# Optimization experiments

Hardware: AMD Instinct MI355X
Metric: run time of the kernel (lower is better)

Reference implementation:

```python
import jax, jax.numpy as jnp
import numpy as np

D = 1024
E = 8
K = 2
NUM_ITER = 2
DT = 0.1
H = 64           # controller_hidden
CTX = 2 * D


def _gelu(t):
    return jax.nn.gelu(t, approximate=False)


def _inl(ctrl, x, v, mu):
    # ctrl: [T, 3D] -> alpha, beta, gate chunks of size D
    alpha_raw, beta_raw, gate_raw = jnp.split(ctrl, 3, axis=-1)
    alpha = jax.nn.sigmoid(alpha_raw)
    beta = jax.nn.softplus(beta_raw)
    gate = jax.nn.sigmoid(gate_raw)
    error = x - mu
    v_next = alpha * v - beta * error
    x_next = x + DT * gate * v_next
    return x_next, v_next


def setup_inputs() -> dict:
    key = jax.random.key(0)
    ks = jax.random.split(key, 20)
    s = 0.02
    inp = {
        'x': jax.random.normal(ks[0], (4, 4096, D), jnp.float32),
        # router MLP
        'w_r1': jax.random.normal(ks[1], (D, D // 4), jnp.float32) * s,
        'b_r1': jnp.zeros((D // 4,), jnp.float32),
        'w_r2': jax.random.normal(ks[2], (D // 4, E), jnp.float32) * s,
        'b_r2': jnp.zeros((E,), jnp.float32),
        # halt gate MLP
        'w_h1': jax.random.normal(ks[3], (D, D // 4), jnp.float32) * s,
        'b_h1': jnp.zeros((D // 4,), jnp.float32),
        'w_h2': jax.random.normal(ks[4], (D // 4, 1), jnp.float32) * s,
        'b_h2': jnp.zeros((1,), jnp.float32),
        # expert tables
        'expert_w1': jax.random.normal(ks[5], (E, CTX, H), jnp.float32) * s,
        'expert_b1': jnp.zeros((E, H), jnp.float32),
        'expert_w2': jax.random.normal(ks[6], (E, H, 3 * D), jnp.float32) * s,
        'expert_b2': jnp.zeros((E, 3 * D), jnp.float32),
        # shared expert
        'w_s1': jax.random.normal(ks[7], (CTX, H), jnp.float32) * s,
        'b_s1': jnp.zeros((H,), jnp.float32),
        'w_s2': jax.random.normal(ks[8], (H, 3 * D), jnp.float32) * s,
        'b_s2': jnp.zeros((3 * D,), jnp.float32),
        'shared_weight': jnp.asarray(0.5, jnp.float32),
        # refine MLP
        'w_f1': jax.random.normal(ks[9], (D, 2 * D), jnp.float32) * s,
        'b_f1': jnp.zeros((2 * D,), jnp.float32),
        'w_f2': jax.random.normal(ks[10], (2 * D, D), jnp.float32) * s,
        'b_f2': jnp.zeros((D,), jnp.float32),
        'integration_weight': jnp.full((D,), 0.5, jnp.float32),
        'mu': jnp.zeros((D,), jnp.float32),
    }
    return inp


def reference(x, w_r1, b_r1, w_r2, b_r2, w_h1, b_h1, w_h2, b_h2,
              expert_w1, expert_b1, expert_w2, expert_b2,
              w_s1, b_s1, w_s2, b_s2, shared_weight,
              w_f1, b_f1, w_f2, b_f2, integration_weight, mu):
    B, N, Dm = x.shape
    xf = x.reshape(B * N, Dm)                       # [T, D]

    # router: top-k over softmax probs, renormalized
    logits = _gelu(xf @ w_r1 + b_r1) @ w_r2 + b_r2  # [T, E]
    probs = jax.nn.softmax(logits, axis=-1)
    top_p, top_i = jax.lax.top_k(probs, K)          # [T, K]
    top_p = top_p / jnp.sum(top_p, axis=-1, keepdims=True)

    flat_idx = top_i.reshape(-1)                    # [T*K]
    flat_w = top_p.reshape(-1, 1)                   # [T*K, 1]

    v = jnp.zeros_like(xf)
    integrated = xf
    for _ in range(NUM_ITER):
        ctx = jnp.concatenate([integrated, v], axis=-1)     # [T, 2D]

        # shared expert path
        shared_ctrl = _gelu(ctx @ w_s1 + b_s1) @ w_s2 + b_s2
        x_shared, v_shared = _inl(shared_ctrl, integrated, v, mu)
        sw = jax.nn.sigmoid(shared_weight)

        # routed experts: gather per-token weights, per-token matvec
        ctx_e = jnp.repeat(ctx, K, axis=0)                  # [T*K, 2D]
        x_e = jnp.repeat(integrated, K, axis=0)
        v_e = jnp.repeat(v, K, axis=0)
        w1 = expert_w1[flat_idx]                            # [T*K, 2D, H]
        b1 = expert_b1[flat_idx]
        w2 = expert_w2[flat_idx]                            # [T*K, H, 3D]
        b2 = expert_b2[flat_idx]
        hidden = _gelu(jnp.einsum('tc,tch->th', ctx_e, w1) + b1)
        ctrl = jnp.einsum('th,tho->to', hidden, w2) + b2    # [T*K, 3D]
        x_r, v_r = _inl(ctrl, x_e, v_e, mu)
        x_r = (x_r * flat_w).reshape(B * N, K, Dm).sum(axis=1)
        v_r = (v_r * flat_w).reshape(B * N, K, Dm).sum(axis=1)

        x_next = sw * x_shared + (1.0 - sw) * x_r
        v_next = sw * v_shared + (1.0 - sw) * v_r

        halt = jax.nn.sigmoid(_gelu(x_next @ w_h1 + b_h1) @ w_h2 + b_h2)  # [T,1]
        refined = _gelu(x_next @ w_f1 + b_f1) @ w_f2 + b_f2               # [T,D]
        integrated = integrated + halt * refined * integration_weight
        v = v_next

    return integrated.reshape(B, N, Dm)
```

## Files before the change

kernel.cpp:

```cpp
#include <hip/hip_runtime.h>


#define TOK   16384
#define DDIM  1024
#define NEXP  8
#define DTC   0.1f
#define NDESC 160

using f32x4 = __attribute__((ext_vector_type(4))) float;
using bfv8  = __attribute__((ext_vector_type(8))) short;

__device__ __forceinline__ unsigned short f2bf(float x){
  unsigned u = __builtin_bit_cast(unsigned, x);
  u += 0x7fffu + ((u >> 16) & 1u);
  return (unsigned short)(u >> 16);
}
__device__ __forceinline__ float bf2f(unsigned short h){
  return __builtin_bit_cast(float, ((unsigned)h) << 16);
}
__device__ __forceinline__ float geluf(float x){
  return 0.5f * x * (1.0f + erff(x * 0.7071067811865476f));
}
__device__ __forceinline__ float sigmf(float x){ return 1.0f/(1.0f+__expf(-x)); }
__device__ __forceinline__ float softpf(float x){
  return fmaxf(x, 0.0f) + __logf(1.0f + __expf(-fabsf(x)));
}
__device__ __forceinline__ f32x4 mfma16(bfv8 a, bfv8 b, f32x4 c){
  return __builtin_amdgcn_mfma_f32_16x16x32_bf16(a, b, c, 0, 0, 0);
}
typedef __attribute__((address_space(1))) const void gvoid_t;
typedef __attribute__((address_space(3))) void svoid_t;
__device__ __forceinline__ void gload16(const void* g, void* l){
  __builtin_amdgcn_global_load_lds((gvoid_t*)g, (svoid_t*)l, 16, 0, 0);
}

__global__ __launch_bounds__(256) void transpose_cast(
    const float* __restrict__ src, unsigned short* __restrict__ dst, int R, int C)
{
  __shared__ float tile[32][33];
  size_t bo = (size_t)blockIdx.z * R * C;
  const float* s = src + bo;
  unsigned short* d = dst + bo;
  int c0 = blockIdx.x * 32, r0 = blockIdx.y * 32;
  int tx = threadIdx.x, ty = threadIdx.y;
  #pragma unroll
  for (int j = 0; j < 4; j++)
    tile[ty + 8*j][tx] = s[(size_t)(r0 + ty + 8*j) * C + c0 + tx];
  __syncthreads();
  #pragma unroll
  for (int j = 0; j < 4; j++)
    d[(size_t)(c0 + ty + 8*j) * R + r0 + tx] = f2bf(tile[tx][ty + 8*j]);
}

__global__ __launch_bounds__(256) void ctx_k(
    const float* __restrict__ outf, unsigned short* __restrict__ ctx)
{
  const int n = TOK * 256;
  for (int i = blockIdx.x * 256 + threadIdx.x; i < n; i += gridDim.x * 256) {
    int t = i >> 8, c4 = (i & 255) * 4;
    float4 xi = ((const float4*)outf)[i];
    ushort4 xb = {f2bf(xi.x), f2bf(xi.y), f2bf(xi.z), f2bf(xi.w)};
    *(ushort4*)&ctx[(size_t)t*2048 + c4] = xb;
    *(ushort4*)&ctx[(size_t)t*2048 + 1024 + c4] = ushort4{0,0,0,0};
  }
}

template<int EPI>
__global__ __launch_bounds__(256) void gemm_k(
    const unsigned short* __restrict__ A, int lda,
    const unsigned short* __restrict__ BT,
    const float* __restrict__ bias, const float* __restrict__ bias2,
    int Kd, int N,
    unsigned short* __restrict__ obf, unsigned short* __restrict__ obf2,
    const float* __restrict__ halt, const float* __restrict__ iw,
    float* __restrict__ integ, unsigned short* __restrict__ ctxX)
{
  __shared__ unsigned short As[128][64];
  __shared__ unsigned short Bs[128][64];
  const int total = gridDim.x * gridDim.y;
  const int bid = blockIdx.y * gridDim.x + blockIdx.x;
  const int swz = (bid & 7) * (total >> 3) + (bid >> 3);
  const int bx = swz % gridDim.x, by = swz / gridDim.x;

  const int tid  = threadIdx.x, lane = tid & 63, w = tid >> 6;
  const int wm   = w >> 1, wn = w & 1;
  const int gm0  = by * 128, gn0 = bx * 128;
  const int r8   = lane >> 3;
  const int sseg = (lane & 7) ^ r8;

  const unsigned short* aga[4];
  const unsigned short* bga[4];
  #pragma unroll
  for (int c = 0; c < 4; c++) {
    aga[c] = A  + (size_t)(gm0 + w*32 + c*8 + r8) * lda + sseg*8;
    bga[c] = BT + (size_t)(gn0 + w*32 + c*8 + r8) * Kd  + sseg*8;
  }

  f32x4 acc[4][4];
  #pragma unroll
  for (int i = 0; i < 4; i++)
    #pragma unroll
    for (int j = 0; j < 4; j++)
      acc[i][j] = f32x4{0.f,0.f,0.f,0.f};

  const int xr = (lane & 7) << 3;
  for (int k0 = 0; k0 < Kd; k0 += 64) {
    #pragma unroll
    for (int c = 0; c < 4; c++) gload16(aga[c] + k0, &As[w*32 + c*8][0]);
    #pragma unroll
    for (int c = 0; c < 4; c++) gload16(bga[c] + k0, &Bs[w*32 + c*8][0]);
    __syncthreads();
    #pragma unroll
    for (int kk = 0; kk < 64; kk += 32) {
      const int kof = kk + ((lane >> 4) << 3);
      bfv8 a[4], b[4];
      #pragma unroll
      for (int mf = 0; mf < 4; mf++)
        a[mf] = *(const bfv8*)&As[wm*64 + mf*16 + (lane & 15)][kof ^ xr];
      #pragma unroll
      for (int nf = 0; nf < 4; nf++)
        b[nf] = *(const bfv8*)&Bs[wn*64 + nf*16 + (lane & 15)][kof ^ xr];
      #pragma unroll
      for (int mf = 0; mf < 4; mf++)
        #pragma unroll
        for (int nf = 0; nf < 4; nf++)
          acc[mf][nf] = mfma16(a[mf], b[nf], acc[mf][nf]);
    }
    __syncthreads();
  }

  #pragma unroll
  for (int mf = 0; mf < 4; mf++) {
    #pragma unroll
    for (int nf = 0; nf < 4; nf++) {
      int col = gn0 + wn*64 + nf*16 + (lane & 15);
      float bc;
      if (EPI == 2) bc = (col < 2048) ? bias[col] : bias2[col - 2048];
      else          bc = bias[col];
      #pragma unroll
      for (int r = 0; r < 4; r++) {
        int row = gm0 + wm*64 + mf*16 + ((lane >> 4) << 2) + r;
        float v = acc[mf][nf][r] + bc;
        if (EPI == 0) {
          obf[(size_t)row * N + col] = f2bf(geluf(v));
        } else if (EPI == 2) {
          if (col < 2048) obf [(size_t)row * 2048 + col]        = f2bf(geluf(v));
          else            obf2[(size_t)row * 256 + (col - 2048)] = f2bf(geluf(v));
        } else {
          size_t ix = (size_t)row * DDIM + col;
          float nv = integ[ix] + halt[row] * v * iw[col];
          integ[ix] = nv;
          ctxX[(size_t)row * 2048 + col] = f2bf(nv);
        }
      }
    }
  }
}

__global__ __launch_bounds__(256) void router_k(
    const unsigned short* __restrict__ h1, const float* __restrict__ w_r2,
    const float* __restrict__ b_r2, int* __restrict__ topi, float* __restrict__ topw)
{
  int t = blockIdx.x * 4 + (threadIdx.x >> 6);
  int lane = threadIdx.x & 63;
  const unsigned short* hp = h1 + (size_t)t * 256 + lane * 4;
  float hv[4];
  #pragma unroll
  for (int j = 0; j < 4; j++) hv[j] = bf2f(hp[j]);
  float acc[8];
  #pragma unroll
  for (int e = 0; e < 8; e++) acc[e] = 0.f;
  #pragma unroll
  for (int j = 0; j < 4; j++) {
    const float* wr = w_r2 + (size_t)(lane*4 + j) * 8;
    #pragma unroll
    for (int e = 0; e < 8; e++) acc[e] += hv[j] * wr[e];
  }
  #pragma unroll
  for (int off = 32; off > 0; off >>= 1)
    #pragma unroll
    for (int e = 0; e < 8; e++) acc[e] += __shfl_xor(acc[e], off);
  if (lane == 0) {
    float lg[8];
    #pragma unroll
    for (int e = 0; e < 8; e++) lg[e] = acc[e] + b_r2[e];
    int i0 = 0; float m0 = lg[0];
    #pragma unroll
    for (int e = 1; e < 8; e++) if (lg[e] > m0) { m0 = lg[e]; i0 = e; }
    int i1 = -1; float m1 = -3.4e38f;
    #pragma unroll
    for (int e = 0; e < 8; e++) if (e != i0 && lg[e] > m1) { m1 = lg[e]; i1 = e; }
    float w0 = 1.0f / (1.0f + expf(m1 - m0));
    topi[t*2] = i0; topi[t*2+1] = i1;
    topw[t*2] = w0; topw[t*2+1] = 1.0f - w0;
  }
}

__global__ __launch_bounds__(256) void haltgate_k(
    const unsigned short* __restrict__ h1, const float* __restrict__ w_h2,
    const float* __restrict__ b_h2, float* __restrict__ halt)
{
  int t = blockIdx.x * 4 + (threadIdx.x >> 6);
  int lane = threadIdx.x & 63;
  const unsigned short* hp = h1 + (size_t)t * 256 + lane * 4;
  float s = 0.f;
  #pragma unroll
  for (int j = 0; j < 4; j++) s += bf2f(hp[j]) * w_h2[lane*4 + j];
  #pragma unroll
  for (int off = 32; off > 0; off >>= 1) s += __shfl_xor(s, off);
  if (lane == 0) halt[t] = sigmf(s + b_h2[0]);
}

__global__ __launch_bounds__(256) void pairb_k(
    const int* __restrict__ topi, const float* __restrict__ topw,
    int* __restrict__ cnt, int* __restrict__ plist, float* __restrict__ wA)
{
  int t = blockIdx.x * 256 + threadIdx.x;
  int a = topi[2*t], b = topi[2*t+1];
  float wa = topw[2*t];
  if (a > b) { int tmp = a; a = b; b = tmp; wa = 1.0f - wa; }
  int pid = a * 8 + b;
  int pos = atomicAdd(&cnt[pid], 1);
  plist[pid * TOK + pos] = t;
  wA[t] = wa;
}

__global__ void desc_k(const int* __restrict__ cnt, int4* __restrict__ desc,
                       int* __restrict__ ndesc)
{
  if (threadIdx.x == 0 && blockIdx.x == 0) {
    int nt = 0, hb = 0;
    for (int p = 0; p < 64; p++) {
      int c = cnt[p];
      for (int o = 0; o < c; o += 128) {
        int rem = c - o; if (rem > 128) rem = 128;
        desc[nt] = make_int4(p, o, rem, hb);
        nt++; hb += 384;
      }
    }
    ndesc[0] = nt;
  }
}

__global__ __launch_bounds__(256) void exp1p_k(
    const unsigned short* __restrict__ ctx,
    const int4* __restrict__ desc, const int* __restrict__ ndesc,
    const int* __restrict__ plist,
    const unsigned short* __restrict__ ew1T, const float* __restrict__ eb1,
    const unsigned short* __restrict__ ws1T, const float* __restrict__ bs1,
    unsigned short* __restrict__ hiddenG)
{
  __shared__ unsigned short As[128][64];
  __shared__ unsigned short Bs[64][64];
  __shared__ int s_tok[128];
  if (blockIdx.x >= ndesc[0]) return;
  int4 dd = desc[blockIdx.x];
  const int pid = dd.x, goff = dd.y, cnt = dd.z, hbase = dd.w;
  const int path = blockIdx.y;
  const int ep = (path == 0) ? (pid >> 3) : (pid & 7);
  const unsigned short* w1 = (path < 2) ? ew1T + (size_t)ep * 64 * 2048 : ws1T;
  const float* b1 = (path < 2) ? eb1 + ep * 64 : bs1;
  const int tid = threadIdx.x, lane = tid & 63, w = tid >> 6;

  if (tid < 128)
    s_tok[tid] = (tid < cnt) ? plist[pid * TOK + goff + tid] : 0;
  __syncthreads();

  const int arow = w*8 + (lane >> 3);
  const int sseg = (lane & 7) ^ (lane >> 3);
  const unsigned short* asrc[4];
  #pragma unroll
  for (int q = 0; q < 4; q++)
    asrc[q] = ctx + (size_t)s_tok[q*32 + arow] * 2048 + sseg * 8;
  const unsigned short* bsrc[2];
  #pragma unroll
  for (int q = 0; q < 2; q++)
    bsrc[q] = w1 + (size_t)(q*32 + arow) * 2048 + sseg * 8;

  f32x4 acc[2][4];
  #pragma unroll
  for (int i = 0; i < 2; i++)
    #pragma unroll
    for (int j = 0; j < 4; j++)
      acc[i][j] = f32x4{0.f,0.f,0.f,0.f};

  const int xr = (lane & 7) << 3;
  for (int k0 = 0; k0 < 2048; k0 += 64) {
    #pragma unroll
    for (int q = 0; q < 4; q++) gload16(asrc[q] + k0, &As[q*32 + w*8][0]);
    #pragma unroll
    for (int q = 0; q < 2; q++) gload16(bsrc[q] + k0, &Bs[q*32 + w*8][0]);
    __syncthreads();
    #pragma unroll
    for (int kk = 0; kk < 64; kk += 32) {
      const int kof = kk + ((lane >> 4) << 3);
      bfv8 a[2], b[4];
      #pragma unroll
      for (int mf = 0; mf < 2; mf++)
        a[mf] = *(const bfv8*)&As[w*32 + mf*16 + (lane & 15)][kof ^ xr];
      #pragma unroll
      for (int nf = 0; nf < 4; nf++)
        b[nf] = *(const bfv8*)&Bs[nf*16 + (lane & 15)][kof ^ xr];
      #pragma unroll
      for (int mf = 0; mf < 2; mf++)
        #pragma unroll
        for (int nf = 0; nf < 4; nf++)
          acc[mf][nf] = mfma16(a[mf], b[nf], acc[mf][nf]);
    }
    __syncthreads();
  }

  #pragma unroll
  for (int mf = 0; mf < 2; mf++) {
    #pragma unroll
    for (int nf = 0; nf < 4; nf++) {
      int col = nf*16 + (lane & 15);
      float bb = b1[col];
      #pragma unroll
      for (int r = 0; r < 4; r++) {
        int row = w*32 + mf*16 + ((lane >> 4) << 2) + r;
        hiddenG[(size_t)(hbase + path*128 + row) * 64 + col] =
            f2bf(geluf(acc[mf][nf][r] + bb));
      }
    }
  }
}

__global__ __launch_bounds__(256) void exp2p_k(
    const unsigned short* __restrict__ hiddenG,
    const int4* __restrict__ desc, const int* __restrict__ ndesc,
    const int* __restrict__ plist, const float* __restrict__ wA,
    const unsigned short* __restrict__ ew2T, const float* __restrict__ eb2,
    const unsigned short* __restrict__ ws2T, const float* __restrict__ bs2,
    const float* __restrict__ swp, const float* __restrict__ mu,
    unsigned short* __restrict__ ctx, unsigned short* __restrict__ xaccB)
{
  __shared__ unsigned short Hs[192][64];
  __shared__ unsigned short W2s[192][64];
  __shared__ int   s_tok[64];
  __shared__ float s_w[64];
  if (blockIdx.x >= ndesc[0]) return;
  int4 dd = desc[blockIdx.x];
  const int pid = dd.x, goff = dd.y, cnt = dd.z, hbase = dd.w;
  const int rhf = blockIdx.y;
  const int cnth = cnt - rhf * 64;
  if (cnth <= 0) return;
  const int e0 = pid >> 3, e1 = pid & 7;
  const int tid = threadIdx.x, lane = tid & 63, w = tid >> 6;
  const float sw = sigmf(swp[0]);

  if (tid < 64) {
    int gr = rhf*64 + tid;
    int tok = 0; float wa = 0.f;
    if (gr < cnt) { tok = plist[pid * TOK + goff + gr]; wa = wA[tok]; }
    s_tok[tid] = tok; s_w[tid] = wa;
  }
  const int srow = w*8 + (lane >> 3);
  const int sseg = (lane & 7) ^ (lane >> 3);
  #pragma unroll
  for (int q = 0; q < 6; q++) {
    int row = q*32 + srow;
    gload16(hiddenG + (size_t)(hbase + (row >> 6)*128 + rhf*64 + (row & 63))*64 + sseg*8,
            &Hs[q*32 + w*8][0]);
  }
  __syncthreads();

  const int xr = (lane & 7) << 3;
  const unsigned short* w2b[3] = { ew2T + (size_t)e0*3072*64,
                                   ew2T + (size_t)e1*3072*64, ws2T };
  const float* b2b[3] = { eb2 + e0*3072, eb2 + e1*3072, bs2 };

  for (int dcq = 0; dcq < 4; dcq++) {
    const int d00 = blockIdx.z * 256 + dcq * 64;
    float xx[4][4], vv[4][4], vtot[4][4], gvtot[4][4];
    int   toks[4]; float cwa[4];
    #pragma unroll
    for (int r = 0; r < 4; r++) {
      int row = w*16 + ((lane >> 4) << 2) + r;
      toks[r] = s_tok[row]; cwa[r] = s_w[row];
      #pragma unroll
      for (int cf = 0; cf < 4; cf++) {
        int d = d00 + cf*16 + (lane & 15);
        xx[cf][r] = bf2f(ctx[(size_t)toks[r]*2048 + d]);
        vv[cf][r] = bf2f(ctx[(size_t)toks[r]*2048 + 1024 + d]);
        vtot[cf][r] = 0.f; gvtot[cf][r] = 0.f;
      }
    }
    #pragma unroll
    for (int path = 0; path < 3; path++) {
      #pragma unroll
      for (int q = 0; q < 6; q++) {
        int row  = q*32 + srow;
        int grow = (row >> 6)*1024 + d00 + (row & 63);
        gload16(w2b[path] + (size_t)grow*64 + sseg*8, &W2s[q*32 + w*8][0]);
      }
      __syncthreads();
      bfv8 a[2];
      #pragma unroll
      for (int kk = 0; kk < 2; kk++)
        a[kk] = *(const bfv8*)&Hs[path*64 + w*16 + (lane & 15)]
                               [(kk*32 + ((lane >> 4) << 3)) ^ xr];
      f32x4 acc[12];
      #pragma unroll
      for (int j = 0; j < 12; j++) acc[j] = f32x4{0.f,0.f,0.f,0.f};
      #pragma unroll
      for (int kk = 0; kk < 2; kk++) {
        const int kof = kk*32 + ((lane >> 4) << 3);
        #pragma unroll
        for (int nf = 0; nf < 12; nf++) {
          bfv8 b = *(const bfv8*)&W2s[nf*16 + (lane & 15)][kof ^ xr];
          acc[nf] = mfma16(a[kk], b, acc[nf]);
        }
      }
      const float* b2 = b2b[path];
      #pragma unroll
      for (int cf = 0; cf < 4; cf++) {
        int d = d00 + cf*16 + (lane & 15);
        float ba = b2[d], bb = b2[1024 + d], bg = b2[2048 + d];
        float muv = mu[d];
        #pragma unroll
        for (int r = 0; r < 4; r++) {
          float cw = (path == 0) ? (1.f - sw) * cwa[r]
                   : (path == 1) ? (1.f - sw) * (1.f - cwa[r]) : sw;
          float al = sigmf(acc[cf][r] + ba);
          float be = softpf(acc[4 + cf][r] + bb);
          float ga = sigmf(acc[8 + cf][r] + bg);
          float vn = al * vv[cf][r] - be * (xx[cf][r] - muv);
          vtot[cf][r]  += cw * vn;
          gvtot[cf][r] += cw * ga * vn;
        }
      }
      __syncthreads();
    }
    #pragma unroll
    for (int r = 0; r < 4; r++) {
      int row = w*16 + ((lane >> 4) << 2) + r;
      if (row >= cnth) continue;
      int tok = toks[r];
      #pragma unroll
      for (int cf = 0; cf < 4; cf++) {
        int d = d00 + cf*16 + (lane & 15);
        xaccB[(size_t)tok*1024 + d]        = f2bf(xx[cf][r] + DTC * gvtot[cf][r]);
        ctx[(size_t)tok*2048 + 1024 + d]   = f2bf(vtot[cf][r]);
      }
    }
  }
}

extern "C" void kernel_launch(void* const* d_in, const int* in_sizes, int n_in,
                              void* d_out, int out_size, void* d_ws, size_t ws_size,
                              hipStream_t stream)
{
  const float* x    = (const float*)d_in[0];
  const float* w_r1 = (const float*)d_in[1];
  const float* b_r1 = (const float*)d_in[2];
  const float* w_r2 = (const float*)d_in[3];
  const float* b_r2 = (const float*)d_in[4];
  const float* w_h1 = (const float*)d_in[5];
  const float* b_h1 = (const float*)d_in[6];
  const float* w_h2 = (const float*)d_in[7];
  const float* b_h2 = (const float*)d_in[8];
  const float* ew1  = (const float*)d_in[9];
  const float* eb1  = (const float*)d_in[10];
  const float* ew2  = (const float*)d_in[11];
  const float* eb2  = (const float*)d_in[12];
  const float* w_s1 = (const float*)d_in[13];
  const float* b_s1 = (const float*)d_in[14];
  const float* w_s2 = (const float*)d_in[15];
  const float* b_s2 = (const float*)d_in[16];
  const float* swt  = (const float*)d_in[17];
  const float* w_f1 = (const float*)d_in[18];
  const float* b_f1 = (const float*)d_in[19];
  const float* w_f2 = (const float*)d_in[20];
  const float* b_f2 = (const float*)d_in[21];
  const float* iw   = (const float*)d_in[22];
  const float* mu   = (const float*)d_in[23];
  float* out = (float*)d_out;

  char* ws = (char*)d_ws;
  size_t off = 0;
  auto take = [&](size_t bytes) -> char* {
    char* p = ws + off;
    off = (off + bytes + 255) & ~(size_t)255;
    return p;
  };
  const size_t TD4 = (size_t)TOK * DDIM * 4;
  unsigned short* xaccB = (unsigned short*)take((size_t)TOK * 1024 * 2);
  unsigned short* ctx   = (unsigned short*)take((size_t)TOK * 2048 * 2);
  unsigned short* rh    = (unsigned short*)take((size_t)TOK * 2048 * 2);
  unsigned short* hiddenG = (unsigned short*)take((size_t)NDESC * 384 * 64 * 2);
  unsigned short* h1 = (unsigned short*)take((size_t)TOK * 256 * 2);
  float* halt = (float*)take((size_t)TOK * 4);
  int*   topi = (int*)take((size_t)TOK * 2 * 4);
  float* topw = (float*)take((size_t)TOK * 2 * 4);
  int*   cnt  = (int*)take(64 * 4);
  int*   ndsc = (int*)take(64);
  int4*  desc = (int4*)take((size_t)NDESC * 16);
  int*   plist= (int*)take((size_t)64 * TOK * 4);
  float* wAa  = (float*)take((size_t)TOK * 4);
  unsigned short* w_r1T = (unsigned short*)take((size_t)256 * 1024 * 2);
  unsigned short* wFH   = (unsigned short*)take((size_t)2304 * 1024 * 2);
  unsigned short* w_f2T = (unsigned short*)take((size_t)1024 * 2048 * 2);
  unsigned short* w_s1T = (unsigned short*)take((size_t)64 * 2048 * 2);
  unsigned short* w_s2T = (unsigned short*)take((size_t)3072 * 64 * 2);
  unsigned short* ew1T  = (unsigned short*)take((size_t)NEXP * 64 * 2048 * 2);
  unsigned short* ew2T  = (unsigned short*)take((size_t)NEXP * 3072 * 64 * 2);
  if (off > ws_size) return;

  hipMemcpyAsync(out, x, TD4, hipMemcpyDeviceToDevice, stream);
  hipMemsetAsync(cnt, 0, 64 * 4, stream);

  dim3 tb(32, 8);
  transpose_cast<<<dim3(  8, 32, 1), tb, 0, stream>>>(w_r1, w_r1T, 1024,  256);
  transpose_cast<<<dim3( 64, 32, 1), tb, 0, stream>>>(w_f1, wFH, 1024, 2048);
  transpose_cast<<<dim3(  8, 32, 1), tb, 0, stream>>>(w_h1, wFH + (size_t)2048*1024, 1024, 256);
  transpose_cast<<<dim3( 32, 64, 1), tb, 0, stream>>>(w_f2, w_f2T, 2048, 1024);
  transpose_cast<<<dim3(  2, 64, 1), tb, 0, stream>>>(w_s1, w_s1T, 2048,   64);
  transpose_cast<<<dim3( 96,  2, 1), tb, 0, stream>>>(w_s2, w_s2T,   64, 3072);
  transpose_cast<<<dim3(  2, 64, 8), tb, 0, stream>>>(ew1,  ew1T,  2048,   64);
  transpose_cast<<<dim3( 96,  2, 8), tb, 0, stream>>>(ew2,  ew2T,    64, 3072);

  ctx_k<<<2048, 256, 0, stream>>>(out, ctx);
  gemm_k<0><<<dim3(2, 128), 256, 0, stream>>>(
      ctx, 2048, w_r1T, b_r1, nullptr, 1024, 256, h1, nullptr,
      nullptr, nullptr, nullptr, nullptr);
  router_k<<<TOK / 4, 256, 0, stream>>>(h1, w_r2, b_r2, topi, topw);
  pairb_k<<<TOK / 256, 256, 0, stream>>>(topi, topw, cnt, plist, wAa);
  desc_k<<<1, 64, 0, stream>>>(cnt, desc, ndsc);

  for (int it = 0; it < 2; it++) {
    exp1p_k<<<dim3(NDESC, 3), 256, 0, stream>>>(
        ctx, desc, ndsc, plist, ew1T, eb1, w_s1T, b_s1, hiddenG);
    exp2p_k<<<dim3(NDESC, 2, 4), 256, 0, stream>>>(
        hiddenG, desc, ndsc, plist, wAa, ew2T, eb2, w_s2T, b_s2,
        swt, mu, ctx, xaccB);
    gemm_k<2><<<dim3(18, 128), 256, 0, stream>>>(
        xaccB, 1024, wFH, b_f1, b_h1, 1024, 2304, rh, h1,
        nullptr, nullptr, nullptr, nullptr);
    haltgate_k<<<TOK / 4, 256, 0, stream>>>(h1, w_h2, b_h2, halt);
    gemm_k<1><<<dim3(8, 128), 256, 0, stream>>>(
        rh, 2048, w_f2T, b_f2, nullptr, 2048, 1024, nullptr, nullptr,
        halt, iw, out, ctx);
  }
}
```

Before: 1.149 ms.

## Store expert context in pair-grouped padded order and restructure expert kernels

```diff
diff --git a/kernel.cpp b/kernel.cpp
--- a/kernel.cpp
+++ b/kernel.cpp
@@ -5,7 +5,8 @@
 #define DDIM  1024
 #define NEXP  8
 #define DTC   0.1f
-#define NDESC 160
+#define NDESC 320
+#define GPAD  20480
 
 using f32x4 = __attribute__((ext_vector_type(4))) float;
 using bfv8  = __attribute__((ext_vector_type(8))) short;
@@ -52,16 +53,33 @@
     d[(size_t)(c0 + ty + 8*j) * R + r0 + tx] = f2bf(tile[tx][ty + 8*j]);
 }
 
-__global__ __launch_bounds__(256) void ctx_k(
-    const float* __restrict__ outf, unsigned short* __restrict__ ctx)
+__global__ __launch_bounds__(256) void xinit_k(
+    const float* __restrict__ xf, unsigned short* __restrict__ xb)
 {
   const int n = TOK * 256;
   for (int i = blockIdx.x * 256 + threadIdx.x; i < n; i += gridDim.x * 256) {
-    int t = i >> 8, c4 = (i & 255) * 4;
-    float4 xi = ((const float4*)outf)[i];
-    ushort4 xb = {f2bf(xi.x), f2bf(xi.y), f2bf(xi.z), f2bf(xi.w)};
-    *(ushort4*)&ctx[(size_t)t*2048 + c4] = xb;
-    *(ushort4*)&ctx[(size_t)t*2048 + 1024 + c4] = ushort4{0,0,0,0};
+    float4 f = ((const float4*)xf)[i];
+    ushort4 u = {f2bf(f.x), f2bf(f.y), f2bf(f.z), f2bf(f.w)};
+    ((ushort4*)xb)[i] = u;
+  }
+}
+
+__global__ __launch_bounds__(256) void ctxb_k(
+    const float* __restrict__ xf, const int* __restrict__ tokmap,
+    unsigned short* __restrict__ ctx)
+{
+  const int g = blockIdx.x, tid = threadIdx.x;
+  const int t = tokmap[g];
+  if (tid < 128) {
+    if (t >= 0) {
+      const float4* s = (const float4*)(xf + (size_t)t * 1024) + tid * 2;
+      float4 f0 = s[0], f1 = s[1];
+      unsigned short tmp[8] = {f2bf(f0.x), f2bf(f0.y), f2bf(f0.z), f2bf(f0.w),
+                               f2bf(f1.x), f2bf(f1.y), f2bf(f1.z), f2bf(f1.w)};
+      *(uint4*)&ctx[(size_t)g * 2048 + tid * 8] = *(uint4*)tmp;
+    }
+  } else {
+    *(uint4*)&ctx[(size_t)g * 2048 + 1024 + (tid - 128) * 8] = uint4{0,0,0,0};
   }
 }
 
@@ -73,7 +91,8 @@
     int Kd, int N,
     unsigned short* __restrict__ obf, unsigned short* __restrict__ obf2,
     const float* __restrict__ halt, const float* __restrict__ iw,
-    float* __restrict__ integ, unsigned short* __restrict__ ctxX)
+    float* __restrict__ integ, unsigned short* __restrict__ ctxX,
+    const int* __restrict__ pf)
 {
   __shared__ unsigned short As[128][64];
   __shared__ unsigned short Bs[128][64];
@@ -150,7 +169,7 @@
           size_t ix = (size_t)row * DDIM + col;
           float nv = integ[ix] + halt[row] * v * iw[col];
           integ[ix] = nv;
-          ctxX[(size_t)row * 2048 + col] = f2bf(nv);
+          ctxX[(size_t)pf[row] * 2048 + col] = f2bf(nv);
         }
       }
     }
@@ -226,110 +245,109 @@
 }
 
 __global__ void desc_k(const int* __restrict__ cnt, int4* __restrict__ desc,
-                       int* __restrict__ ndesc)
+                       int* __restrict__ ndesc, int* __restrict__ pbase)
 {
   if (threadIdx.x == 0 && blockIdx.x == 0) {
-    int nt = 0, hb = 0;
+    int nt = 0, rb = 0;
     for (int p = 0; p < 64; p++) {
+      pbase[p] = rb;
       int c = cnt[p];
-      for (int o = 0; o < c; o += 128) {
-        int rem = c - o; if (rem > 128) rem = 128;
-        desc[nt] = make_int4(p, o, rem, hb);
-        nt++; hb += 384;
-      }
+      for (int o = 0; o < c; o += 64) {
+        int rem = c - o; if (rem > 64) rem = 64;
+        desc[nt] = make_int4(p, rb + o, rem, 0);
+        nt++;
+      }
+      rb += (c + 63) & ~63;
     }
     ndesc[0] = nt;
+  }
+}
+
+__global__ __launch_bounds__(256) void pmap_k(
+    const int* __restrict__ cnt, const int* __restrict__ pbase,
+    const int* __restrict__ plist, int* __restrict__ tokmap, int* __restrict__ pf)
+{
+  int pid = blockIdx.x;
+  int pos = blockIdx.y * 256 + threadIdx.x;
+  if (pos < cnt[pid]) {
+    int t = plist[pid * TOK + pos];
+    int g = pbase[pid] + pos;
+    tokmap[g] = t;
+    pf[t] = g;
   }
 }
 
 __global__ __launch_bounds__(256) void exp1p_k(
     const unsigned short* __restrict__ ctx,
     const int4* __restrict__ desc, const int* __restrict__ ndesc,
-    const int* __restrict__ plist,
     const unsigned short* __restrict__ ew1T, const float* __restrict__ eb1,
     const unsigned short* __restrict__ ws1T, const float* __restrict__ bs1,
     unsigned short* __restrict__ hiddenG)
 {
-  __shared__ unsigned short As[128][64];
+  __shared__ unsigned short As[64][64];
   __shared__ unsigned short Bs[64][64];
-  __shared__ int s_tok[128];
-  if (blockIdx.x >= ndesc[0]) return;
-  int4 dd = desc[blockIdx.x];
-  const int pid = dd.x, goff = dd.y, cnt = dd.z, hbase = dd.w;
-  const int path = blockIdx.y;
+  const int nb = gridDim.x;
+  const int vb = (blockIdx.x & 7) * (nb >> 3) + (blockIdx.x >> 3);
+  const int dx = vb / 3, path = vb - dx * 3;
+  if (dx >= ndesc[0]) return;
+  int4 dd = desc[dx];
+  const int pid = dd.x, rbt = dd.y;
   const int ep = (path == 0) ? (pid >> 3) : (pid & 7);
   const unsigned short* w1 = (path < 2) ? ew1T + (size_t)ep * 64 * 2048 : ws1T;
   const float* b1 = (path < 2) ? eb1 + ep * 64 : bs1;
   const int tid = threadIdx.x, lane = tid & 63, w = tid >> 6;
 
-  if (tid < 128)
-    s_tok[tid] = (tid < cnt) ? plist[pid * TOK + goff + tid] : 0;
-  __syncthreads();
-
   const int arow = w*8 + (lane >> 3);
   const int sseg = (lane & 7) ^ (lane >> 3);
-  const unsigned short* asrc[4];
-  #pragma unroll
-  for (int q = 0; q < 4; q++)
-    asrc[q] = ctx + (size_t)s_tok[q*32 + arow] * 2048 + sseg * 8;
+  const unsigned short* asrc[2];
   const unsigned short* bsrc[2];
   #pragma unroll
-  for (int q = 0; q < 2; q++)
-    bsrc[q] = w1 + (size_t)(q*32 + arow) * 2048 + sseg * 8;
-
-  f32x4 acc[2][4];
-  #pragma unroll
-  for (int i = 0; i < 2; i++)
-    #pragma unroll
-    for (int j = 0; j < 4; j++)
-      acc[i][j] = f32x4{0.f,0.f,0.f,0.f};
+  for (int q = 0; q < 2; q++) {
+    asrc[q] = ctx + (size_t)(rbt + q*32 + arow) * 2048 + sseg * 8;
+    bsrc[q] = w1  + (size_t)(q*32 + arow) * 2048 + sseg * 8;
+  }
+
+  f32x4 acc[4];
+  #pragma unroll
+  for (int j = 0; j < 4; j++) acc[j] = f32x4{0.f,0.f,0.f,0.f};
 
   const int xr = (lane & 7) << 3;
   for (int k0 = 0; k0 < 2048; k0 += 64) {
     #pragma unroll
-    for (int q = 0; q < 4; q++) gload16(asrc[q] + k0, &As[q*32 + w*8][0]);
+    for (int q = 0; q < 2; q++) gload16(asrc[q] + k0, &As[q*32 + w*8][0]);
     #pragma unroll
     for (int q = 0; q < 2; q++) gload16(bsrc[q] + k0, &Bs[q*32 + w*8][0]);
     __syncthreads();
     #pragma unroll
     for (int kk = 0; kk < 64; kk += 32) {
       const int kof = kk + ((lane >> 4) << 3);
-      bfv8 a[2], b[4];
-      #pragma unroll
-      for (int mf = 0; mf < 2; mf++)
-        a[mf] = *(const bfv8*)&As[w*32 + mf*16 + (lane & 15)][kof ^ xr];
-      #pragma unroll
-      for (int nf = 0; nf < 4; nf++)
-        b[nf] = *(const bfv8*)&Bs[nf*16 + (lane & 15)][kof ^ xr];
-      #pragma unroll
-      for (int mf = 0; mf < 2; mf++)
-        #pragma unroll
-        for (int nf = 0; nf < 4; nf++)
-          acc[mf][nf] = mfma16(a[mf], b[nf], acc[mf][nf]);
+      bfv8 a = *(const bfv8*)&As[w*16 + (lane & 15)][kof ^ xr];
+      #pragma unroll
+      for (int nf = 0; nf < 4; nf++) {
+        bfv8 b = *(const bfv8*)&Bs[nf*16 + (lane & 15)][kof ^ xr];
+        acc[nf] = mfma16(a, b, acc[nf]);
+      }
     }
     __syncthreads();
   }
 
   #pragma unroll
-  for (int mf = 0; mf < 2; mf++) {
-    #pragma unroll
-    for (int nf = 0; nf < 4; nf++) {
-      int col = nf*16 + (lane & 15);
-      float bb = b1[col];
-      #pragma unroll
-      for (int r = 0; r < 4; r++) {
-        int row = w*32 + mf*16 + ((lane >> 4) << 2) + r;
-        hiddenG[(size_t)(hbase + path*128 + row) * 64 + col] =
-            f2bf(geluf(acc[mf][nf][r] + bb));
-      }
-    }
-  }
-}
-
-__global__ __launch_bounds__(256) void exp2p_k(
+  for (int nf = 0; nf < 4; nf++) {
+    int col = nf*16 + (lane & 15);
+    float bb = b1[col];
+    #pragma unroll
+    for (int r = 0; r < 4; r++) {
+      int row = w*16 + ((lane >> 4) << 2) + r;
+      hiddenG[(size_t)(3*rbt + path*64 + row) * 64 + col] =
+          f2bf(geluf(acc[nf][r] + bb));
+    }
+  }
+}
+
+__global__ __launch_bounds__(256, 3) void exp2p_k(
     const unsigned short* __restrict__ hiddenG,
     const int4* __restrict__ desc, const int* __restrict__ ndesc,
-    const int* __restrict__ plist, const float* __restrict__ wA,
+    const int* __restrict__ tokmap, const float* __restrict__ wA,
     const unsigned short* __restrict__ ew2T, const float* __restrict__ eb2,
     const unsigned short* __restrict__ ws2T, const float* __restrict__ bs2,
     const float* __restrict__ swp, const float* __restrict__ mu,
@@ -339,67 +357,60 @@
   __shared__ unsigned short W2s[192][64];
   __shared__ int   s_tok[64];
   __shared__ float s_w[64];
-  if (blockIdx.x >= ndesc[0]) return;
-  int4 dd = desc[blockIdx.x];
-  const int pid = dd.x, goff = dd.y, cnt = dd.z, hbase = dd.w;
-  const int rhf = blockIdx.y;
-  const int cnth = cnt - rhf * 64;
-  if (cnth <= 0) return;
+  const int nb = gridDim.x;
+  const int vb = (blockIdx.x & 7) * (nb >> 3) + (blockIdx.x >> 3);
+  const int dx = vb >> 2, zq = vb & 3;
+  if (dx >= ndesc[0]) return;
+  int4 dd = desc[dx];
+  const int pid = dd.x, rbt = dd.y, cnt = dd.z;
   const int e0 = pid >> 3, e1 = pid & 7;
   const int tid = threadIdx.x, lane = tid & 63, w = tid >> 6;
   const float sw = sigmf(swp[0]);
 
   if (tid < 64) {
-    int gr = rhf*64 + tid;
-    int tok = 0; float wa = 0.f;
-    if (gr < cnt) { tok = plist[pid * TOK + goff + gr]; wa = wA[tok]; }
-    s_tok[tid] = tok; s_w[tid] = wa;
+    int t = tokmap[rbt + tid];
+    if (t < 0) t = 0;
+    s_tok[tid] = t; s_w[tid] = wA[t];
   }
   const int srow = w*8 + (lane >> 3);
   const int sseg = (lane & 7) ^ (lane >> 3);
   #pragma unroll
-  for (int q = 0; q < 6; q++) {
-    int row = q*32 + srow;
-    gload16(hiddenG + (size_t)(hbase + (row >> 6)*128 + rhf*64 + (row & 63))*64 + sseg*8,
+  for (int q = 0; q < 6; q++)
+    gload16(hiddenG + (size_t)(3*rbt + q*32 + srow) * 64 + sseg*8,
             &Hs[q*32 + w*8][0]);
-  }
-  __syncthreads();
-
-  const int xr = (lane & 7) << 3;
   const unsigned short* w2b[3] = { ew2T + (size_t)e0*3072*64,
                                    ew2T + (size_t)e1*3072*64, ws2T };
   const float* b2b[3] = { eb2 + e0*3072, eb2 + e1*3072, bs2 };
+  const int d0q = zq * 256;
+  #pragma unroll
+  for (int q = 0; q < 6; q++) {
+    int row = q*32 + srow;
+    int grow = (row >> 6)*1024 + d0q + (row & 63);
+    gload16(w2b[0] + (size_t)grow*64 + sseg*8, &W2s[q*32 + w*8][0]);
+  }
+  __syncthreads();
+
+  const int xr  = (lane & 7) << 3;
+  const int cr4 = (lane >> 4) << 2;
+  int toks[4]; float wa4[4];
+  #pragma unroll
+  for (int r = 0; r < 4; r++) {
+    int row = w*16 + cr4 + r;
+    toks[r] = s_tok[row]; wa4[r] = s_w[row];
+  }
 
   for (int dcq = 0; dcq < 4; dcq++) {
-    const int d00 = blockIdx.z * 256 + dcq * 64;
-    float xx[4][4], vv[4][4], vtot[4][4], gvtot[4][4];
-    int   toks[4]; float cwa[4];
-    #pragma unroll
-    for (int r = 0; r < 4; r++) {
-      int row = w*16 + ((lane >> 4) << 2) + r;
-      toks[r] = s_tok[row]; cwa[r] = s_w[row];
-      #pragma unroll
-      for (int cf = 0; cf < 4; cf++) {
-        int d = d00 + cf*16 + (lane & 15);
-        xx[cf][r] = bf2f(ctx[(size_t)toks[r]*2048 + d]);
-        vv[cf][r] = bf2f(ctx[(size_t)toks[r]*2048 + 1024 + d]);
-        vtot[cf][r] = 0.f; gvtot[cf][r] = 0.f;
-      }
+    const int d00 = d0q + dcq*64;
+    f32x4 A4[4], B4[4], C4[4], D4[4];
+    #pragma unroll
+    for (int cf = 0; cf < 4; cf++) {
+      A4[cf] = f32x4{0.f,0.f,0.f,0.f}; B4[cf] = f32x4{0.f,0.f,0.f,0.f};
+      C4[cf] = f32x4{0.f,0.f,0.f,0.f}; D4[cf] = f32x4{0.f,0.f,0.f,0.f};
     }
     #pragma unroll
     for (int path = 0; path < 3; path++) {
-      #pragma unroll
-      for (int q = 0; q < 6; q++) {
-        int row  = q*32 + srow;
-        int grow = (row >> 6)*1024 + d00 + (row & 63);
-        gload16(w2b[path] + (size_t)grow*64 + sseg*8, &W2s[q*32 + w*8][0]);
-      }
-      __syncthreads();
-      bfv8 a[2];
-      #pragma unroll
-      for (int kk = 0; kk < 2; kk++)
-        a[kk] = *(const bfv8*)&Hs[path*64 + w*16 + (lane & 15)]
-                               [(kk*32 + ((lane >> 4) << 3)) ^ xr];
+      bfv8 a0 = *(const bfv8*)&Hs[path*64 + w*16 + (lane & 15)][(((lane>>4)<<3)) ^ xr];
+      bfv8 a1 = *(const bfv8*)&Hs[path*64 + w*16 + (lane & 15)][(32 + ((lane>>4)<<3)) ^ xr];
       f32x4 acc[12];
       #pragma unroll
       for (int j = 0; j < 12; j++) acc[j] = f32x4{0.f,0.f,0.f,0.f};
@@ -409,7 +420,20 @@
         #pragma unroll
         for (int nf = 0; nf < 12; nf++) {
           bfv8 b = *(const bfv8*)&W2s[nf*16 + (lane & 15)][kof ^ xr];
-          acc[nf] = mfma16(a[kk], b, acc[nf]);
+          acc[nf] = mfma16(kk == 0 ? a0 : a1, b, acc[nf]);
+        }
+      }
+      __syncthreads();
+      const int pc = dcq*3 + path;
+      if (pc < 11) {
+        const int npath = (path + 1 == 3) ? 0 : path + 1;
+        const int nd00  = d0q + (dcq + (path == 2)) * 64;
+        const unsigned short* nw2 = w2b[npath];
+        #pragma unroll
+        for (int q = 0; q < 6; q++) {
+          int row = q*32 + srow;
+          int grow = (row >> 6)*1024 + nd00 + (row & 63);
+          gload16(nw2 + (size_t)grow*64 + sseg*8, &W2s[q*32 + w*8][0]);
         }
       }
       const float* b2 = b2b[path];
@@ -417,32 +441,39 @@
       for (int cf = 0; cf < 4; cf++) {
         int d = d00 + cf*16 + (lane & 15);
         float ba = b2[d], bb = b2[1024 + d], bg = b2[2048 + d];
-        float muv = mu[d];
         #pragma unroll
         for (int r = 0; r < 4; r++) {
-          float cw = (path == 0) ? (1.f - sw) * cwa[r]
-                   : (path == 1) ? (1.f - sw) * (1.f - cwa[r]) : sw;
+          float cw = (path == 0) ? (1.f - sw) * wa4[r]
+                   : (path == 1) ? (1.f - sw) * (1.f - wa4[r]) : sw;
           float al = sigmf(acc[cf][r] + ba);
           float be = softpf(acc[4 + cf][r] + bb);
           float ga = sigmf(acc[8 + cf][r] + bg);
-          float vn = al * vv[cf][r] - be * (xx[cf][r] - muv);
-          vtot[cf][r]  += cw * vn;
-          gvtot[cf][r] += cw * ga * vn;
+          A4[cf][r] += cw * al;       B4[cf][r] += cw * be;
+          C4[cf][r] += cw * ga * al;  D4[cf][r] += cw * ga * be;
         }
       }
+      if (path == 2) {
+        #pragma unroll
+        for (int cf = 0; cf < 4; cf++) {
+          int d = d00 + cf*16 + (lane & 15);
+          float muv = mu[d];
+          #pragma unroll
+          for (int r = 0; r < 4; r++) {
+            int row = w*16 + cr4 + r;
+            size_t g = (size_t)(rbt + row);
+            float xx = bf2f(ctx[g*2048 + d]);
+            float vv = bf2f(ctx[g*2048 + 1024 + d]);
+            float err = xx - muv;
+            float vt = vv * A4[cf][r] - err * B4[cf][r];
+            float gv = vv * C4[cf][r] - err * D4[cf][r];
+            if (row < cnt) {
+              xaccB[(size_t)toks[r]*1024 + d] = f2bf(xx + DTC * gv);
+              ctx[g*2048 + 1024 + d]          = f2bf(vt);
+            }
+          }
+        }
+      }
       __syncthreads();
-    }
-    #pragma unroll
-    for (int r = 0; r < 4; r++) {
-      int row = w*16 + ((lane >> 4) << 2) + r;
-      if (row >= cnth) continue;
-      int tok = toks[r];
-      #pragma unroll
-      for (int cf = 0; cf < 4; cf++) {
-        int d = d00 + cf*16 + (lane & 15);
-        xaccB[(size_t)tok*1024 + d]        = f2bf(xx[cf][r] + DTC * gvtot[cf][r]);
-        ctx[(size_t)tok*2048 + 1024 + d]   = f2bf(vtot[cf][r]);
-      }
     }
   }
 }
@@ -486,18 +517,21 @@
   };
   const size_t TD4 = (size_t)TOK * DDIM * 4;
   unsigned short* xaccB = (unsigned short*)take((size_t)TOK * 1024 * 2);
-  unsigned short* ctx   = (unsigned short*)take((size_t)TOK * 2048 * 2);
+  unsigned short* ctx   = (unsigned short*)take((size_t)GPAD * 2048 * 2);
   unsigned short* rh    = (unsigned short*)take((size_t)TOK * 2048 * 2);
-  unsigned short* hiddenG = (unsigned short*)take((size_t)NDESC * 384 * 64 * 2);
+  unsigned short* hiddenG = (unsigned short*)take((size_t)3 * GPAD * 64 * 2);
   unsigned short* h1 = (unsigned short*)take((size_t)TOK * 256 * 2);
   float* halt = (float*)take((size_t)TOK * 4);
   int*   topi = (int*)take((size_t)TOK * 2 * 4);
   float* topw = (float*)take((size_t)TOK * 2 * 4);
   int*   cnt  = (int*)take(64 * 4);
   int*   ndsc = (int*)take(64);
+  int*   pbase= (int*)take(64 * 4);
   int4*  desc = (int4*)take((size_t)NDESC * 16);
   int*   plist= (int*)take((size_t)64 * TOK * 4);
   float* wAa  = (float*)take((size_t)TOK * 4);
+  int*   tokmap = (int*)take((size_t)GPAD * 4);
+  int*   pf     = (int*)take((size_t)TOK * 4);
   unsigned short* w_r1T = (unsigned short*)take((size_t)256 * 1024 * 2);
   unsigned short* wFH   = (unsigned short*)take((size_t)2304 * 1024 * 2);
   unsigned short* w_f2T = (unsigned short*)take((size_t)1024 * 2048 * 2);
@@ -509,6 +543,7 @@
 
   hipMemcpyAsync(out, x, TD4, hipMemcpyDeviceToDevice, stream);
   hipMemsetAsync(cnt, 0, 64 * 4, stream);
+  hipMemsetAsync(tokmap, 0xFF, (size_t)GPAD * 4, stream);
 
   dim3 tb(32, 8);
   transpose_cast<<<dim3(  8, 32, 1), tb, 0, stream>>>(w_r1, w_r1T, 1024,  256);
@@ -520,26 +555,28 @@
   transpose_cast<<<dim3(  2, 64, 8), tb, 0, stream>>>(ew1,  ew1T,  2048,   64);
   transpose_cast<<<dim3( 96,  2, 8), tb, 0, stream>>>(ew2,  ew2T,    64, 3072);
 
-  ctx_k<<<2048, 256, 0, stream>>>(out, ctx);
+  xinit_k<<<2048, 256, 0, stream>>>(x, xaccB);
   gemm_k<0><<<dim3(2, 128), 256, 0, stream>>>(
-      ctx, 2048, w_r1T, b_r1, nullptr, 1024, 256, h1, nullptr,
-      nullptr, nullptr, nullptr, nullptr);
+      xaccB, 1024, w_r1T, b_r1, nullptr, 1024, 256, h1, nullptr,
+      nullptr, nullptr, nullptr, nullptr, nullptr);
   router_k<<<TOK / 4, 256, 0, stream>>>(h1, w_r2, b_r2, topi, topw);
   pairb_k<<<TOK / 256, 256, 0, stream>>>(topi, topw, cnt, plist, wAa);
-  desc_k<<<1, 64, 0, stream>>>(cnt, desc, ndsc);
+  desc_k<<<1, 64, 0, stream>>>(cnt, desc, ndsc, pbase);
+  pmap_k<<<dim3(64, 64), 256, 0, stream>>>(cnt, pbase, plist, tokmap, pf);
+  ctxb_k<<<GPAD, 256, 0, stream>>>(out, tokmap, ctx);
 
   for (int it = 0; it < 2; it++) {
-    exp1p_k<<<dim3(NDESC, 3), 256, 0, stream>>>(
-        ctx, desc, ndsc, plist, ew1T, eb1, w_s1T, b_s1, hiddenG);
-    exp2p_k<<<dim3(NDESC, 2, 4), 256, 0, stream>>>(
-        hiddenG, desc, ndsc, plist, wAa, ew2T, eb2, w_s2T, b_s2,
-        swt, mu, ctx, xaccB);
+    exp1p_k<<<960, 256, 0, stream>>>(ctx, desc, ndsc,
+                                     ew1T, eb1, w_s1T, b_s1, hiddenG);
+    exp2p_k<<<1280, 256, 0, stream>>>(hiddenG, desc, ndsc, tokmap, wAa,
+                                      ew2T, eb2, w_s2T, b_s2, swt, mu,
+                                      ctx, xaccB);
     gemm_k<2><<<dim3(18, 128), 256, 0, stream>>>(
         xaccB, 1024, wFH, b_f1, b_h1, 1024, 2304, rh, h1,
-        nullptr, nullptr, nullptr, nullptr);
+        nullptr, nullptr, nullptr, nullptr, nullptr);
     haltgate_k<<<TOK / 4, 256, 0, stream>>>(h1, w_h2, b_h2, halt);
     gemm_k<1><<<dim3(8, 128), 256, 0, stream>>>(
         rh, 2048, w_f2T, b_f2, nullptr, 2048, 1024, nullptr, nullptr,
-        halt, iw, out, ctx);
-  }
-}
+        halt, iw, out, ctx, pf);
+  }
+}
```

After: 1.893 ms. 1.65x slower.
